# Optimization experiments

Measured on AMD Instinct MI355X. Metric: run time of the kernel, lower is better.

## Reference

```python
import jax, jax.numpy as jnp
import numpy as np

B, S, D = 2, 2048, 4096
H, KV, HD = 32, 8, 128          # query heads, kv heads, head_dim
N_REP = H // KV                 # GQA groups = 4
ROPE_THETA = 1000000.0


def setup_inputs() -> dict:
    key = jax.random.key(0)
    ks = jax.random.split(key, 8)
    s = 0.02
    return {
        "hidden_states": jax.random.normal(ks[0], (B, S, D), jnp.float32),
        "position_ids": jnp.broadcast_to(jnp.arange(S, dtype=jnp.int32)[None, :], (B, S)),
        "wq": jax.random.normal(ks[1], (D, H * HD), jnp.float32) * s,
        "bq": jax.random.normal(ks[2], (H * HD,), jnp.float32) * s,
        "wk": jax.random.normal(ks[3], (D, KV * HD), jnp.float32) * s,
        "bk": jax.random.normal(ks[4], (KV * HD,), jnp.float32) * s,
        "wv": jax.random.normal(ks[5], (D, KV * HD), jnp.float32) * s,
        "bv": jax.random.normal(ks[6], (KV * HD,), jnp.float32) * s,
        "wo": jax.random.normal(ks[7], (H * HD, D), jnp.float32) * s,
    }


def _rope_cos_sin(position_ids, head_dim, theta):
    pos = position_ids.astype(jnp.float32)
    dim = head_dim // 2
    freqs = 1.0 / theta ** (jnp.arange(0, dim, dtype=jnp.float32) / dim)
    t = pos[..., None] * freqs[None, None, :]          # [B,S,dim]
    return jnp.cos(t)[..., None, :], jnp.sin(t)[..., None, :]  # [B,S,1,dim]


def _apply_rope(x, cos, sin):
    half = x.shape[-1] // 2
    x1, x2 = x[..., :half], x[..., half:]
    return jnp.concatenate([x1 * cos - x2 * sin, x1 * sin + x2 * cos], axis=-1)


def reference(hidden_states, position_ids, wq, bq, wk, bk, wv, bv, wo):
    q = (hidden_states @ wq + bq).reshape(B, S, H, HD)
    k = (hidden_states @ wk + bk).reshape(B, S, KV, HD)
    v = (hidden_states @ wv + bv).reshape(B, S, KV, HD)

    cos, sin = _rope_cos_sin(position_ids, HD, ROPE_THETA)
    q = _apply_rope(q, cos, sin)
    k = _apply_rope(k, cos, sin)

    # GQA: physically expand KV heads (adjacent repeats, matches repeat_kv)
    k = jnp.repeat(k, N_REP, axis=2)   # [B,S,H,HD]
    v = jnp.repeat(v, N_REP, axis=2)

    # causal bias (attention_mask defaults to all-ones, so only causal matters)
    neg = jnp.finfo(jnp.float32).min
    causal = jnp.tril(jnp.ones((S, S), dtype=bool))
    bias = jnp.where(causal, 0.0, neg).astype(jnp.float32)  # [S,S]

    scale = 1.0 / jnp.sqrt(jnp.float32(HD))
    scores = jnp.einsum("bqhd,bkhd->bhqk", q * scale, k) + bias[None, None]
    attn = jax.nn.softmax(scores, axis=-1)                  # [B,H,S,S]
    out = jnp.einsum("bhqk,bkhd->bqhd", attn, v)
    out = out.reshape(B, S, H * HD)
    return out @ wo
```

## Files before the change

kernel.cpp:

```cpp
#include <hip/hip_runtime.h>
#include <hip/hip_bf16.h>
#include <math.h>


typedef __bf16 bf16;
typedef __attribute__((ext_vector_type(8))) __bf16 bf16x8;
typedef __attribute__((ext_vector_type(4))) float f32x4;

__device__ __forceinline__ void glds16(const void* g, void* l) {
    __builtin_amdgcn_global_load_lds(
        (const __attribute__((address_space(1))) void*)g,
        (__attribute__((address_space(3))) void*)l, 16, 0, 0);
}

__global__ __launch_bounds__(256) void convert_kernel(
    const float* __restrict__ in, bf16* __restrict__ out)
{
    const size_t i0 = ((size_t)blockIdx.x * 256 + threadIdx.x) * 8;
    const float4 a = *(const float4*)(in + i0);
    const float4 b = *(const float4*)(in + i0 + 4);
    bf16x8 p;
    p[0] = (bf16)a.x; p[1] = (bf16)a.y; p[2] = (bf16)a.z; p[3] = (bf16)a.w;
    p[4] = (bf16)b.x; p[5] = (bf16)b.y; p[6] = (bf16)b.z; p[7] = (bf16)b.w;
    *(bf16x8*)(out + i0) = p;
}

__global__ __launch_bounds__(256) void transpose_conv_kernel(
    const float* __restrict__ in, bf16* __restrict__ out, int N)
{
    __shared__ bf16 tile[32 * 68];
    const int n0 = blockIdx.x * 32, k0 = blockIdx.y * 64;
    const int t = threadIdx.x;
    const int nn = t & 31, kk0 = (t >> 5) * 8;
#pragma unroll
    for (int j = 0; j < 8; ++j)
        tile[nn * 68 + kk0 + j] = (bf16)in[(size_t)(k0 + kk0 + j) * N + n0 + nn];
    __syncthreads();
    const int n2 = t >> 3, c = (t & 7) * 8;
    *(bf16x8*)(out + (size_t)(n0 + n2) * 4096 + k0 + c) = *(const bf16x8*)(&tile[n2 * 68 + c]);
}

template <int EPI, int AF32>
__global__ __launch_bounds__(256) void gemm_kernel(
    const float* __restrict__ A_f32, const bf16* __restrict__ A_bf16,
    const bf16* __restrict__ BqT, const bf16* __restrict__ BkT, const bf16* __restrict__ BvT,
    const float* __restrict__ b_q, const float* __restrict__ b_k, const float* __restrict__ b_v,
    bf16* __restrict__ q_out, bf16* __restrict__ kv_k, bf16* __restrict__ kv_v,
    float* __restrict__ f_out)
{
    constexpr int LDA = AF32 ? 34 : 32;
    __shared__ bf16 As[128 * LDA];
    __shared__ bf16 Bs[128 * 32];

    const int nt = blockIdx.x, mt = blockIdx.y;
    const int tid = threadIdx.x;
    const int wave = tid >> 6, lane = tid & 63;
    const int l15 = lane & 15, quad = lane >> 4;
    const int wm = (wave >> 1) * 64, wn = (wave & 1) * 64;

    const bf16* BT;
    const float* bias = nullptr;
    int sel = 0, ncol0;
    if (EPI == 0) {
        if (nt < 32)      { BT = BqT; bias = b_q; sel = 0; ncol0 = nt * 128; }
        else if (nt < 40) { BT = BkT; bias = b_k; sel = 1; ncol0 = (nt - 32) * 128; }
        else              { BT = BvT; bias = b_v; sel = 2; ncol0 = (nt - 40) * 128; }
    } else {
        BT = BqT; ncol0 = nt * 128;
    }
    const int row0 = mt * 128;

    const f32x4 vzero = {0.f, 0.f, 0.f, 0.f};
    f32x4 acc[4][4];
#pragma unroll
    for (int mi = 0; mi < 4; ++mi)
#pragma unroll
        for (int ni = 0; ni < 4; ++ni) acc[mi][ni] = vzero;

    const int a_row = tid >> 1, a_seg = (tid & 1) * 16;
    const int g_row = lane >> 2, g_seg = (lane & 3) * 8;

    for (int k0 = 0; k0 < 4096; k0 += 32) {
        if (AF32) {
            const float4* src = (const float4*)(A_f32 + (size_t)(row0 + a_row) * 4096 + k0 + a_seg);
            float4 f0 = src[0], f1 = src[1], f2 = src[2], f3 = src[3];
            bf16x8 p0, p1;
            p0[0] = (bf16)f0.x; p0[1] = (bf16)f0.y; p0[2] = (bf16)f0.z; p0[3] = (bf16)f0.w;
            p0[4] = (bf16)f1.x; p0[5] = (bf16)f1.y; p0[6] = (bf16)f1.z; p0[7] = (bf16)f1.w;
            p1[0] = (bf16)f2.x; p1[1] = (bf16)f2.y; p1[2] = (bf16)f2.z; p1[3] = (bf16)f2.w;
            p1[4] = (bf16)f3.x; p1[5] = (bf16)f3.y; p1[6] = (bf16)f3.z; p1[7] = (bf16)f3.w;
            *(bf16x8*)(&As[a_row * LDA + a_seg]) = p0;
            *(bf16x8*)(&As[a_row * LDA + a_seg + 8]) = p1;
        } else {
#pragma unroll
            for (int c = 0; c < 2; ++c)
                glds16(A_bf16 + (size_t)(row0 + wave * 32 + c * 16 + g_row) * 4096 + k0 + g_seg,
                       &As[(wave * 32 + c * 16) * 32]);
        }
#pragma unroll
        for (int c = 0; c < 2; ++c)
            glds16(BT + (size_t)(ncol0 + wave * 32 + c * 16 + g_row) * 4096 + k0 + g_seg,
                   &Bs[(wave * 32 + c * 16) * 32]);
        __syncthreads();

        bf16x8 af[4], bfv[4];
#pragma unroll
        for (int mi = 0; mi < 4; ++mi)
            af[mi] = *(const bf16x8*)(&As[(wm + mi * 16 + l15) * LDA + quad * 8]);
#pragma unroll
        for (int ni = 0; ni < 4; ++ni)
            bfv[ni] = *(const bf16x8*)(&Bs[(wn + ni * 16 + l15) * 32 + quad * 8]);
#pragma unroll
        for (int mi = 0; mi < 4; ++mi)
#pragma unroll
            for (int ni = 0; ni < 4; ++ni)
                acc[mi][ni] = __builtin_amdgcn_mfma_f32_16x16x32_bf16(af[mi], bfv[ni], acc[mi][ni], 0, 0, 0);
        __syncthreads();
    }

#pragma unroll
    for (int mi = 0; mi < 4; ++mi)
#pragma unroll
        for (int ni = 0; ni < 4; ++ni)
#pragma unroll
            for (int i = 0; i < 4; ++i) {
                const int gr = row0 + wm + mi * 16 + quad * 4 + i;
                const int gc = ncol0 + wn + ni * 16 + l15;
                float vv = acc[mi][ni][i];
                if (EPI == 1) {
                    f_out[(size_t)gr * 4096 + gc] = vv;
                } else {
                    vv += bias[gc];
                    if (sel == 0) {
                        q_out[(size_t)gr * 4096 + gc] = (bf16)vv;
                    } else {
                        bf16* dst = (sel == 1) ? kv_k : kv_v;
                        dst[(size_t)((gr >> 11) * 8 + (gc >> 7)) * 262144 +
                            (size_t)(gr & 2047) * 128 + (gc & 127)] = (bf16)vv;
                    }
                }
            }
}

__global__ __launch_bounds__(256) void rope_q_kernel(
    bf16* __restrict__ q, const int* __restrict__ pos_ids)
{
    const int idx = blockIdx.x * 256 + threadIdx.x;
    const int d = idx & 63, h = (idx >> 6) & 31, tok = idx >> 11;
    const float posv = (float)pos_ids[tok];
    const float fr = exp2f((float)d * (-19.931568569324174f / 64.f));
    float sn, cs;
    sincosf(posv * fr, &sn, &cs);
    bf16* xp = q + (size_t)tok * 4096 + h * 128 + d;
    const float x1 = (float)xp[0], x2 = (float)xp[64];
    const float scale = 0.08838834764831845f;
    xp[0]  = (bf16)((x1 * cs - x2 * sn) * scale);
    xp[64] = (bf16)((x1 * sn + x2 * cs) * scale);
}

__global__ __launch_bounds__(256) void rope_k_kernel(
    bf16* __restrict__ k, const int* __restrict__ pos_ids)
{
    const int idx = blockIdx.x * 256 + threadIdx.x;
    const int d = idx & 63, s = (idx >> 6) & 2047, bk = idx >> 17;
    const int b = bk >> 3;
    const float posv = (float)pos_ids[b * 2048 + s];
    const float fr = exp2f((float)d * (-19.931568569324174f / 64.f));
    float sn, cs;
    sincosf(posv * fr, &sn, &cs);
    bf16* xp = k + ((size_t)bk * 2048 + s) * 128 + d;
    const float x1 = (float)xp[0], x2 = (float)xp[64];
    xp[0]  = (bf16)(x1 * cs - x2 * sn);
    xp[64] = (bf16)(x1 * sn + x2 * cs);
}

__global__ __launch_bounds__(256) void attn_kernel(
    const bf16* __restrict__ q, const bf16* __restrict__ k,
    const bf16* __restrict__ v, bf16* __restrict__ o)
{
    __shared__ bf16 Ksl[64 * 136];
    __shared__ bf16 Vsl[128 * 72];
    __shared__ bf16 Psl[4 * 16 * 68];

    const int pair = blockIdx.x & 7;
    const int h  = (blockIdx.x >> 3) & 31;
    const int b  = blockIdx.x >> 8;
    const int kvh = h >> 2;
    const int tid = threadIdx.x;
    const int wave = tid >> 6, lane = tid & 63;
    const int l15 = lane & 15, quad = lane >> 4;

    const bf16* kbase = k + (size_t)(b * 8 + kvh) * 2048 * 128;
    const bf16* vbase = v + (size_t)(b * 8 + kvh) * 2048 * 128;

    const int kr = tid >> 2, ksg = (tid & 3) * 32;
    const f32x4 vzero = {0.f, 0.f, 0.f, 0.f};

#pragma unroll 1
    for (int phase = 0; phase < 2; ++phase) {
        const int qt = phase ? (15 - pair) : pair;
        const int qbase = qt * 128 + wave * 32;

        bf16x8 qf[2][4];
#pragma unroll
        for (int mi = 0; mi < 2; ++mi) {
            const bf16* qrow = q + ((size_t)(b * 2048 + qbase + mi * 16 + l15) * 32 + h) * 128;
#pragma unroll
            for (int kb = 0; kb < 4; ++kb)
                qf[mi][kb] = *(const bf16x8*)(qrow + kb * 32 + quad * 8);
        }

        f32x4 acc_o[2][8];
#pragma unroll
        for (int mi = 0; mi < 2; ++mi)
#pragma unroll
            for (int i = 0; i < 8; ++i) acc_o[mi][i] = vzero;
        float m_i[2][4], l_i[2][4];
#pragma unroll
        for (int mi = 0; mi < 2; ++mi)
#pragma unroll
            for (int i = 0; i < 4; ++i) { m_i[mi][i] = -INFINITY; l_i[mi][i] = 0.f; }

        const int nT = 2 * qt + 2;
        for (int t = 0; t < nT; ++t) {
            const int kv0 = t * 64;
            {
                const bf16x8* ks = (const bf16x8*)(kbase + (size_t)(kv0 + kr) * 128 + ksg);
                bf16x8* kd = (bf16x8*)(&Ksl[kr * 136 + ksg]);
                kd[0] = ks[0]; kd[1] = ks[1]; kd[2] = ks[2]; kd[3] = ks[3];
            }
            {
                const bf16x8* vs = (const bf16x8*)(vbase + (size_t)(kv0 + lane) * 128 + wave * 32);
                bf16x8 w0 = vs[0], w1 = vs[1], w2 = vs[2], w3 = vs[3];
#pragma unroll
                for (int i = 0; i < 8; ++i) {
                    Vsl[(wave * 32 + i)      * 72 + lane] = w0[i];
                    Vsl[(wave * 32 + 8 + i)  * 72 + lane] = w1[i];
                    Vsl[(wave * 32 + 16 + i) * 72 + lane] = w2[i];
                    Vsl[(wave * 32 + 24 + i) * 72 + lane] = w3[i];
                }
            }
            __syncthreads();

            if (kv0 <= qbase + 31) {
                f32x4 sacc[2][4];
#pragma unroll
                for (int mi = 0; mi < 2; ++mi)
#pragma unroll
                    for (int nt = 0; nt < 4; ++nt) sacc[mi][nt] = vzero;
#pragma unroll
                for (int nt = 0; nt < 4; ++nt)
#pragma unroll
                    for (int kb = 0; kb < 4; ++kb) {
                        const bf16x8 kf = *(const bf16x8*)(&Ksl[(nt * 16 + l15) * 136 + kb * 32 + quad * 8]);
                        sacc[0][nt] = __builtin_amdgcn_mfma_f32_16x16x32_bf16(qf[0][kb], kf, sacc[0][nt], 0, 0, 0);
                        sacc[1][nt] = __builtin_amdgcn_mfma_f32_16x16x32_bf16(qf[1][kb], kf, sacc[1][nt], 0, 0, 0);
                    }

                bf16x8 pf[2][2];
#pragma unroll
                for (int mi = 0; mi < 2; ++mi) {
                    const int rb = qbase + mi * 16;
                    if (kv0 + 63 > rb) {
#pragma unroll
                        for (int nt = 0; nt < 4; ++nt) {
                            const int kvc = kv0 + nt * 16 + l15;
#pragma unroll
                            for (int i = 0; i < 4; ++i)
                                if (kvc > rb + quad * 4 + i) sacc[mi][nt][i] = -INFINITY;
                        }
                    }
                    float mt_[4];
#pragma unroll
                    for (int i = 0; i < 4; ++i)
                        mt_[i] = fmaxf(fmaxf(sacc[mi][0][i], sacc[mi][1][i]),
                                       fmaxf(sacc[mi][2][i], sacc[mi][3][i]));
#pragma unroll
                    for (int off = 1; off < 16; off <<= 1)
#pragma unroll
                        for (int i = 0; i < 4; ++i)
                            mt_[i] = fmaxf(mt_[i], __shfl_xor(mt_[i], off, 64));

                    float alpha[4];
#pragma unroll
                    for (int i = 0; i < 4; ++i) {
                        const float mnew = fmaxf(m_i[mi][i], mt_[i]);
                        alpha[i] = __expf(m_i[mi][i] - mnew);
                        m_i[mi][i] = mnew;
                    }
                    float rs[4] = {0.f, 0.f, 0.f, 0.f};
#pragma unroll
                    for (int nt = 0; nt < 4; ++nt)
#pragma unroll
                        for (int i = 0; i < 4; ++i) {
                            const float pv = __expf(sacc[mi][nt][i] - m_i[mi][i]);
                            rs[i] += pv;
                            Psl[wave * 1088 + (quad * 4 + i) * 68 + nt * 16 + l15] = (bf16)pv;
                        }
#pragma unroll
                    for (int off = 1; off < 16; off <<= 1)
#pragma unroll
                        for (int i = 0; i < 4; ++i)
                            rs[i] += __shfl_xor(rs[i], off, 64);
#pragma unroll
                    for (int i = 0; i < 4; ++i) l_i[mi][i] = l_i[mi][i] * alpha[i] + rs[i];
#pragma unroll
                    for (int dn = 0; dn < 8; ++dn)
#pragma unroll
                        for (int i = 0; i < 4; ++i) acc_o[mi][dn][i] *= alpha[i];
#pragma unroll
                    for (int k2 = 0; k2 < 2; ++k2)
                        pf[mi][k2] = *(const bf16x8*)(&Psl[wave * 1088 + l15 * 68 + k2 * 32 + quad * 8]);
                }

#pragma unroll
                for (int dn = 0; dn < 8; ++dn)
#pragma unroll
                    for (int k2 = 0; k2 < 2; ++k2) {
                        const bf16x8 vf = *(const bf16x8*)(&Vsl[(dn * 16 + l15) * 72 + k2 * 32 + quad * 8]);
                        acc_o[0][dn] = __builtin_amdgcn_mfma_f32_16x16x32_bf16(pf[0][k2], vf, acc_o[0][dn], 0, 0, 0);
                        acc_o[1][dn] = __builtin_amdgcn_mfma_f32_16x16x32_bf16(pf[1][k2], vf, acc_o[1][dn], 0, 0, 0);
                    }
            }
            __syncthreads();
        }

#pragma unroll
        for (int mi = 0; mi < 2; ++mi) {
            float inv[4];
#pragma unroll
            for (int i = 0; i < 4; ++i) inv[i] = 1.f / l_i[mi][i];
#pragma unroll
            for (int dn = 0; dn < 8; ++dn)
#pragma unroll
                for (int i = 0; i < 4; ++i) {
                    const int s = qbase + mi * 16 + quad * 4 + i;
                    o[(((size_t)b * 2048 + s) * 32 + h) * 128 + dn * 16 + l15] =
                        (bf16)(acc_o[mi][dn][i] * inv[i]);
                }
        }
    }
}

extern "C" void kernel_launch(void* const* d_in, const int* in_sizes, int n_in,
                              void* d_out, int out_size, void* d_ws, size_t ws_size,
                              hipStream_t stream)
{
    (void)in_sizes; (void)n_in; (void)out_size;
    const float* hidden = (const float*)d_in[0];
    const int*   pos    = (const int*)d_in[1];
    const float* wq     = (const float*)d_in[2];
    const float* bq_    = (const float*)d_in[3];
    const float* wk     = (const float*)d_in[4];
    const float* bk_    = (const float*)d_in[5];
    const float* wv     = (const float*)d_in[6];
    const float* bv_    = (const float*)d_in[7];
    const float* wo     = (const float*)d_in[8];
    float* out = (float*)d_out;

    char* ws = (char*)d_ws;
    bf16* wqT   = (bf16*)(ws);
    bf16* wkT   = (bf16*)(ws + 33554432);
    bf16* wvT   = (bf16*)(ws + 41943040);
    bf16* q_pre = (bf16*)(ws + 50331648);
    bf16* k_t   = (bf16*)(ws + 83886080);
    bf16* v_t   = (bf16*)(ws + 92274688);
    bf16* hid_b = (bf16*)(ws + 100663296);
    bf16* attn_o = wqT;
    bf16* woT    = q_pre;
    const bool have_hid = (ws_size >= 134217728);

    transpose_conv_kernel<<<dim3(128, 64), 256, 0, stream>>>(wq, wqT, 4096);
    transpose_conv_kernel<<<dim3(32, 64), 256, 0, stream>>>(wk, wkT, 1024);
    transpose_conv_kernel<<<dim3(32, 64), 256, 0, stream>>>(wv, wvT, 1024);

    if (have_hid) {
        convert_kernel<<<8192, 256, 0, stream>>>(hidden, hid_b);
        gemm_kernel<0, 0><<<dim3(48, 32), 256, 0, stream>>>(
            nullptr, hid_b, wqT, wkT, wvT, bq_, bk_, bv_, q_pre, k_t, v_t, nullptr);
    } else {
        gemm_kernel<0, 1><<<dim3(48, 32), 256, 0, stream>>>(
            hidden, nullptr, wqT, wkT, wvT, bq_, bk_, bv_, q_pre, k_t, v_t, nullptr);
    }

    rope_q_kernel<<<32768, 256, 0, stream>>>(q_pre, pos);
    rope_k_kernel<<<8192, 256, 0, stream>>>(k_t, pos);

    attn_kernel<<<512, 256, 0, stream>>>(q_pre, k_t, v_t, attn_o);

    transpose_conv_kernel<<<dim3(128, 64), 256, 0, stream>>>(wo, woT, 4096);

    gemm_kernel<1, 0><<<dim3(32, 32), 256, 0, stream>>>(
        nullptr, attn_o, woT, nullptr, nullptr, nullptr, nullptr, nullptr,
        nullptr, nullptr, nullptr, out);
}
```

Baseline: 921.0 us.

## Double-buffer K/V tiles with register prefetch and fuse both query-tile phases

Measured after the change: 953.6 us. +3.5%, slower.

```diff
diff --git a/kernel.cpp b/kernel.cpp
--- a/kernel.cpp
+++ b/kernel.cpp
@@ -178,9 +178,10 @@
     const bf16* __restrict__ q, const bf16* __restrict__ k,
     const bf16* __restrict__ v, bf16* __restrict__ o)
 {
-    __shared__ bf16 Ksl[64 * 136];
-    __shared__ bf16 Vsl[128 * 72];
-    __shared__ bf16 Psl[4 * 16 * 68];
+    constexpr int KSTR = 138, VSTR = 70, PSTR = 70;
+    __shared__ bf16 Ksl[2][64 * KSTR];
+    __shared__ bf16 Vsl[2][128 * VSTR];
+    __shared__ bf16 Psl[4 * 16 * PSTR];
 
     const int pair = blockIdx.x & 7;
     const int h  = (blockIdx.x >> 3) & 31;
@@ -190,141 +191,40 @@
     const int wave = tid >> 6, lane = tid & 63;
     const int l15 = lane & 15, quad = lane >> 4;
 
+    const int qt0 = pair, qt1 = 15 - pair;
+    const int nT0 = 2 * qt0 + 2, nT = nT0 + 2 * qt1 + 2;
+
     const bf16* kbase = k + (size_t)(b * 8 + kvh) * 2048 * 128;
     const bf16* vbase = v + (size_t)(b * 8 + kvh) * 2048 * 128;
 
     const int kr = tid >> 2, ksg = (tid & 3) * 32;
     const f32x4 vzero = {0.f, 0.f, 0.f, 0.f};
 
-#pragma unroll 1
-    for (int phase = 0; phase < 2; ++phase) {
-        const int qt = phase ? (15 - pair) : pair;
-        const int qbase = qt * 128 + wave * 32;
-
-        bf16x8 qf[2][4];
+    bf16x8 qf[2][4];
+    f32x4 acc_o[2][8];
+    float m_i[2][4], l_i[2][4];
+    int qbase = qt0 * 128 + wave * 32;
+
+    auto load_q = [&](int qt) {
+        const int qb = qt * 128 + wave * 32;
 #pragma unroll
         for (int mi = 0; mi < 2; ++mi) {
-            const bf16* qrow = q + ((size_t)(b * 2048 + qbase + mi * 16 + l15) * 32 + h) * 128;
+            const bf16* qrow = q + ((size_t)(b * 2048 + qb + mi * 16 + l15) * 32 + h) * 128;
 #pragma unroll
             for (int kb = 0; kb < 4; ++kb)
                 qf[mi][kb] = *(const bf16x8*)(qrow + kb * 32 + quad * 8);
         }
-
-        f32x4 acc_o[2][8];
-#pragma unroll
-        for (int mi = 0; mi < 2; ++mi)
+    };
+    auto reset_state = [&]() {
+#pragma unroll
+        for (int mi = 0; mi < 2; ++mi) {
 #pragma unroll
             for (int i = 0; i < 8; ++i) acc_o[mi][i] = vzero;
-        float m_i[2][4], l_i[2][4];
-#pragma unroll
-        for (int mi = 0; mi < 2; ++mi)
 #pragma unroll
             for (int i = 0; i < 4; ++i) { m_i[mi][i] = -INFINITY; l_i[mi][i] = 0.f; }
-
-        const int nT = 2 * qt + 2;
-        for (int t = 0; t < nT; ++t) {
-            const int kv0 = t * 64;
-            {
-                const bf16x8* ks = (const bf16x8*)(kbase + (size_t)(kv0 + kr) * 128 + ksg);
-                bf16x8* kd = (bf16x8*)(&Ksl[kr * 136 + ksg]);
-                kd[0] = ks[0]; kd[1] = ks[1]; kd[2] = ks[2]; kd[3] = ks[3];
-            }
-            {
-                const bf16x8* vs = (const bf16x8*)(vbase + (size_t)(kv0 + lane) * 128 + wave * 32);
-                bf16x8 w0 = vs[0], w1 = vs[1], w2 = vs[2], w3 = vs[3];
-#pragma unroll
-                for (int i = 0; i < 8; ++i) {
-                    Vsl[(wave * 32 + i)      * 72 + lane] = w0[i];
-                    Vsl[(wave * 32 + 8 + i)  * 72 + lane] = w1[i];
-                    Vsl[(wave * 32 + 16 + i) * 72 + lane] = w2[i];
-                    Vsl[(wave * 32 + 24 + i) * 72 + lane] = w3[i];
-                }
-            }
-            __syncthreads();
-
-            if (kv0 <= qbase + 31) {
-                f32x4 sacc[2][4];
-#pragma unroll
-                for (int mi = 0; mi < 2; ++mi)
-#pragma unroll
-                    for (int nt = 0; nt < 4; ++nt) sacc[mi][nt] = vzero;
-#pragma unroll
-                for (int nt = 0; nt < 4; ++nt)
-#pragma unroll
-                    for (int kb = 0; kb < 4; ++kb) {
-                        const bf16x8 kf = *(const bf16x8*)(&Ksl[(nt * 16 + l15) * 136 + kb * 32 + quad * 8]);
-                        sacc[0][nt] = __builtin_amdgcn_mfma_f32_16x16x32_bf16(qf[0][kb], kf, sacc[0][nt], 0, 0, 0);
-                        sacc[1][nt] = __builtin_amdgcn_mfma_f32_16x16x32_bf16(qf[1][kb], kf, sacc[1][nt], 0, 0, 0);
-                    }
-
-                bf16x8 pf[2][2];
-#pragma unroll
-                for (int mi = 0; mi < 2; ++mi) {
-                    const int rb = qbase + mi * 16;
-                    if (kv0 + 63 > rb) {
-#pragma unroll
-                        for (int nt = 0; nt < 4; ++nt) {
-                            const int kvc = kv0 + nt * 16 + l15;
-#pragma unroll
-                            for (int i = 0; i < 4; ++i)
-                                if (kvc > rb + quad * 4 + i) sacc[mi][nt][i] = -INFINITY;
-                        }
-                    }
-                    float mt_[4];
-#pragma unroll
-                    for (int i = 0; i < 4; ++i)
-                        mt_[i] = fmaxf(fmaxf(sacc[mi][0][i], sacc[mi][1][i]),
-                                       fmaxf(sacc[mi][2][i], sacc[mi][3][i]));
-#pragma unroll
-                    for (int off = 1; off < 16; off <<= 1)
-#pragma unroll
-                        for (int i = 0; i < 4; ++i)
-                            mt_[i] = fmaxf(mt_[i], __shfl_xor(mt_[i], off, 64));
-
-                    float alpha[4];
-#pragma unroll
-                    for (int i = 0; i < 4; ++i) {
-                        const float mnew = fmaxf(m_i[mi][i], mt_[i]);
-                        alpha[i] = __expf(m_i[mi][i] - mnew);
-                        m_i[mi][i] = mnew;
-                    }
-                    float rs[4] = {0.f, 0.f, 0.f, 0.f};
-#pragma unroll
-                    for (int nt = 0; nt < 4; ++nt)
-#pragma unroll
-                        for (int i = 0; i < 4; ++i) {
-                            const float pv = __expf(sacc[mi][nt][i] - m_i[mi][i]);
-                            rs[i] += pv;
-                            Psl[wave * 1088 + (quad * 4 + i) * 68 + nt * 16 + l15] = (bf16)pv;
-                        }
-#pragma unroll
-                    for (int off = 1; off < 16; off <<= 1)
-#pragma unroll
-                        for (int i = 0; i < 4; ++i)
-                            rs[i] += __shfl_xor(rs[i], off, 64);
-#pragma unroll
-                    for (int i = 0; i < 4; ++i) l_i[mi][i] = l_i[mi][i] * alpha[i] + rs[i];
-#pragma unroll
-                    for (int dn = 0; dn < 8; ++dn)
-#pragma unroll
-                        for (int i = 0; i < 4; ++i) acc_o[mi][dn][i] *= alpha[i];
-#pragma unroll
-                    for (int k2 = 0; k2 < 2; ++k2)
-                        pf[mi][k2] = *(const bf16x8*)(&Psl[wave * 1088 + l15 * 68 + k2 * 32 + quad * 8]);
-                }
-
-#pragma unroll
-                for (int dn = 0; dn < 8; ++dn)
-#pragma unroll
-                    for (int k2 = 0; k2 < 2; ++k2) {
-                        const bf16x8 vf = *(const bf16x8*)(&Vsl[(dn * 16 + l15) * 72 + k2 * 32 + quad * 8]);
-                        acc_o[0][dn] = __builtin_amdgcn_mfma_f32_16x16x32_bf16(pf[0][k2], vf, acc_o[0][dn], 0, 0, 0);
-                        acc_o[1][dn] = __builtin_amdgcn_mfma_f32_16x16x32_bf16(pf[1][k2], vf, acc_o[1][dn], 0, 0, 0);
-                    }
-            }
-            __syncthreads();
-        }
-
+        }
+    };
+    auto epilogue = [&]() {
 #pragma unroll
         for (int mi = 0; mi < 2; ++mi) {
             float inv[4];
@@ -339,7 +239,138 @@
                         (bf16)(acc_o[mi][dn][i] * inv[i]);
                 }
         }
+    };
+
+    bf16x8 kreg[4], vreg[4];
+    auto issue_loads = [&](int kv0) {
+        const bf16x8* ks = (const bf16x8*)(kbase + (size_t)(kv0 + kr) * 128 + ksg);
+        kreg[0] = ks[0]; kreg[1] = ks[1]; kreg[2] = ks[2]; kreg[3] = ks[3];
+        const bf16x8* vs = (const bf16x8*)(vbase + (size_t)(kv0 + lane) * 128 + wave * 32);
+        vreg[0] = vs[0]; vreg[1] = vs[1]; vreg[2] = vs[2]; vreg[3] = vs[3];
+    };
+    auto write_lds = [&](int buf) {
+        bf16x8* kd = (bf16x8*)(&Ksl[buf][kr * KSTR + ksg]);
+        kd[0] = kreg[0]; kd[1] = kreg[1]; kd[2] = kreg[2]; kd[3] = kreg[3];
+#pragma unroll
+        for (int i = 0; i < 8; ++i) {
+            Vsl[buf][(wave * 32 + i)      * VSTR + lane] = vreg[0][i];
+            Vsl[buf][(wave * 32 + 8 + i)  * VSTR + lane] = vreg[1][i];
+            Vsl[buf][(wave * 32 + 16 + i) * VSTR + lane] = vreg[2][i];
+            Vsl[buf][(wave * 32 + 24 + i) * VSTR + lane] = vreg[3][i];
+        }
+    };
+
+    issue_loads(0);
+    write_lds(0);
+    load_q(qt0);
+    reset_state();
+    __syncthreads();
+
+    int cur = 0;
+    for (int s = 0; s < nT; ++s) {
+        if (s + 1 < nT) {
+            const int nk = (s + 1 < nT0 ? s + 1 : s + 1 - nT0) * 64;
+            issue_loads(nk);
+        }
+        if (s == nT0) {
+            epilogue();
+            load_q(qt1);
+            reset_state();
+            qbase = qt1 * 128 + wave * 32;
+        }
+        const int kv0 = (s < nT0 ? s : s - nT0) * 64;
+
+        if (kv0 <= qbase + 31) {
+            f32x4 sacc[2][4];
+#pragma unroll
+            for (int mi = 0; mi < 2; ++mi)
+#pragma unroll
+                for (int nt = 0; nt < 4; ++nt) sacc[mi][nt] = vzero;
+            __builtin_amdgcn_s_setprio(1);
+#pragma unroll
+            for (int nt = 0; nt < 4; ++nt)
+#pragma unroll
+                for (int kb = 0; kb < 4; ++kb) {
+                    const bf16x8 kf = *(const bf16x8*)(&Ksl[cur][(nt * 16 + l15) * KSTR + kb * 32 + quad * 8]);
+                    sacc[0][nt] = __builtin_amdgcn_mfma_f32_16x16x32_bf16(qf[0][kb], kf, sacc[0][nt], 0, 0, 0);
+                    sacc[1][nt] = __builtin_amdgcn_mfma_f32_16x16x32_bf16(qf[1][kb], kf, sacc[1][nt], 0, 0, 0);
+                }
+            __builtin_amdgcn_s_setprio(0);
+
+            bf16x8 pf[2][2];
+#pragma unroll
+            for (int mi = 0; mi < 2; ++mi) {
+                const int rb = qbase + mi * 16;
+                if (kv0 + 63 > rb) {
+#pragma unroll
+                    for (int nt = 0; nt < 4; ++nt) {
+                        const int kvc = kv0 + nt * 16 + l15;
+#pragma unroll
+                        for (int i = 0; i < 4; ++i)
+                            if (kvc > rb + quad * 4 + i) sacc[mi][nt][i] = -INFINITY;
+                    }
+                }
+                float mt_[4];
+#pragma unroll
+                for (int i = 0; i < 4; ++i)
+                    mt_[i] = fmaxf(fmaxf(sacc[mi][0][i], sacc[mi][1][i]),
+                                   fmaxf(sacc[mi][2][i], sacc[mi][3][i]));
+#pragma unroll
+                for (int off = 1; off < 16; off <<= 1)
+#pragma unroll
+                    for (int i = 0; i < 4; ++i)
+                        mt_[i] = fmaxf(mt_[i], __shfl_xor(mt_[i], off, 64));
+
+                float alpha[4];
+#pragma unroll
+                for (int i = 0; i < 4; ++i) {
+                    const float mnew = fmaxf(m_i[mi][i], mt_[i]);
+                    alpha[i] = __expf(m_i[mi][i] - mnew);
+                    m_i[mi][i] = mnew;
+                }
+                float rs[4] = {0.f, 0.f, 0.f, 0.f};
+#pragma unroll
+                for (int nt = 0; nt < 4; ++nt)
+#pragma unroll
+                    for (int i = 0; i < 4; ++i) {
+                        const float pv = __expf(sacc[mi][nt][i] - m_i[mi][i]);
+                        rs[i] += pv;
+                        Psl[wave * (16 * PSTR) + (quad * 4 + i) * PSTR + nt * 16 + l15] = (bf16)pv;
+                    }
+#pragma unroll
+                for (int off = 1; off < 16; off <<= 1)
+#pragma unroll
+                    for (int i = 0; i < 4; ++i)
+                        rs[i] += __shfl_xor(rs[i], off, 64);
+#pragma unroll
+                for (int i = 0; i < 4; ++i) l_i[mi][i] = l_i[mi][i] * alpha[i] + rs[i];
+#pragma unroll
+                for (int dn = 0; dn < 8; ++dn)
+#pragma unroll
+                    for (int i = 0; i < 4; ++i) acc_o[mi][dn][i] *= alpha[i];
+#pragma unroll
+                for (int k2 = 0; k2 < 2; ++k2)
+                    pf[mi][k2] = *(const bf16x8*)(&Psl[wave * (16 * PSTR) + l15 * PSTR + k2 * 32 + quad * 8]);
+            }
+
+            __builtin_amdgcn_s_setprio(1);
+#pragma unroll
+            for (int dn = 0; dn < 8; ++dn)
+#pragma unroll
+                for (int k2 = 0; k2 < 2; ++k2) {
+                    const bf16x8 vf = *(const bf16x8*)(&Vsl[cur][(dn * 16 + l15) * VSTR + k2 * 32 + quad * 8]);
+                    acc_o[0][dn] = __builtin_amdgcn_mfma_f32_16x16x32_bf16(pf[0][k2], vf, acc_o[0][dn], 0, 0, 0);
+                    acc_o[1][dn] = __builtin_amdgcn_mfma_f32_16x16x32_bf16(pf[1][k2], vf, acc_o[1][dn], 0, 0, 0);
+                }
+            __builtin_amdgcn_s_setprio(0);
+        }
+
+        if (s + 1 < nT) write_lds(cur ^ 1);
+        __syncthreads();
+        cur ^= 1;
     }
+
+    epilogue();
 }
 
 extern "C" void kernel_launch(void* const* d_in, const int* in_sizes, int n_in,
```

## Transpose QK^T MFMA so softmax rows are lane-local, with lazy rescaling

Applied to the files above, without the earlier changes.

Result: faster. 872.5 us (-5.3%).

```diff
diff --git a/kernel.cpp b/kernel.cpp
--- a/kernel.cpp
+++ b/kernel.cpp
@@ -11,6 +11,12 @@
     __builtin_amdgcn_global_load_lds(
         (const __attribute__((address_space(1))) void*)g,
         (__attribute__((address_space(3))) void*)l, 16, 0, 0);
+}
+
+__device__ __forceinline__ unsigned cvt_pk_bf16(float lo, float hi) {
+    unsigned r;
+    asm("v_cvt_pk_bf16_f32 %0, %1, %2" : "=v"(r) : "v"(lo), "v"(hi));
+    return r;
 }
 
 __global__ __launch_bounds__(256) void convert_kernel(
@@ -215,11 +221,8 @@
         for (int mi = 0; mi < 2; ++mi)
 #pragma unroll
             for (int i = 0; i < 8; ++i) acc_o[mi][i] = vzero;
-        float m_i[2][4], l_i[2][4];
-#pragma unroll
-        for (int mi = 0; mi < 2; ++mi)
-#pragma unroll
-            for (int i = 0; i < 4; ++i) { m_i[mi][i] = -INFINITY; l_i[mi][i] = 0.f; }
+        float m_i[2] = {-INFINITY, -INFINITY};
+        float l_i[2] = {0.f, 0.f};
 
         const int nT = 2 * qt + 2;
         for (int t = 0; t < nT; ++t) {
@@ -248,14 +251,16 @@
                 for (int mi = 0; mi < 2; ++mi)
 #pragma unroll
                     for (int nt = 0; nt < 4; ++nt) sacc[mi][nt] = vzero;
+                __builtin_amdgcn_s_setprio(1);
 #pragma unroll
                 for (int nt = 0; nt < 4; ++nt)
 #pragma unroll
                     for (int kb = 0; kb < 4; ++kb) {
                         const bf16x8 kf = *(const bf16x8*)(&Ksl[(nt * 16 + l15) * 136 + kb * 32 + quad * 8]);
-                        sacc[0][nt] = __builtin_amdgcn_mfma_f32_16x16x32_bf16(qf[0][kb], kf, sacc[0][nt], 0, 0, 0);
-                        sacc[1][nt] = __builtin_amdgcn_mfma_f32_16x16x32_bf16(qf[1][kb], kf, sacc[1][nt], 0, 0, 0);
-                    }
+                        sacc[0][nt] = __builtin_amdgcn_mfma_f32_16x16x32_bf16(kf, qf[0][kb], sacc[0][nt], 0, 0, 0);
+                        sacc[1][nt] = __builtin_amdgcn_mfma_f32_16x16x32_bf16(kf, qf[1][kb], sacc[1][nt], 0, 0, 0);
+                    }
+                __builtin_amdgcn_s_setprio(0);
 
                 bf16x8 pf[2][2];
 #pragma unroll
@@ -264,55 +269,62 @@
                     if (kv0 + 63 > rb) {
 #pragma unroll
                         for (int nt = 0; nt < 4; ++nt) {
-                            const int kvc = kv0 + nt * 16 + l15;
+                            const int kvr = kv0 + nt * 16 + quad * 4;
 #pragma unroll
                             for (int i = 0; i < 4; ++i)
-                                if (kvc > rb + quad * 4 + i) sacc[mi][nt][i] = -INFINITY;
+                                if (kvr + i > rb + l15) sacc[mi][nt][i] = -INFINITY;
                         }
                     }
-                    float mt_[4];
-#pragma unroll
-                    for (int i = 0; i < 4; ++i)
-                        mt_[i] = fmaxf(fmaxf(sacc[mi][0][i], sacc[mi][1][i]),
-                                       fmaxf(sacc[mi][2][i], sacc[mi][3][i]));
-#pragma unroll
-                    for (int off = 1; off < 16; off <<= 1)
+                    float tm;
+                    {
+                        f32x4 m4;
 #pragma unroll
                         for (int i = 0; i < 4; ++i)
-                            mt_[i] = fmaxf(mt_[i], __shfl_xor(mt_[i], off, 64));
-
-                    float alpha[4];
-#pragma unroll
-                    for (int i = 0; i < 4; ++i) {
-                        const float mnew = fmaxf(m_i[mi][i], mt_[i]);
-                        alpha[i] = __expf(m_i[mi][i] - mnew);
-                        m_i[mi][i] = mnew;
-                    }
-                    float rs[4] = {0.f, 0.f, 0.f, 0.f};
+                            m4[i] = fmaxf(fmaxf(sacc[mi][0][i], sacc[mi][1][i]),
+                                          fmaxf(sacc[mi][2][i], sacc[mi][3][i]));
+                        tm = fmaxf(fmaxf(m4[0], m4[1]), fmaxf(m4[2], m4[3]));
+                        tm = fmaxf(tm, __shfl_xor(tm, 16, 64));
+                        tm = fmaxf(tm, __shfl_xor(tm, 32, 64));
+                    }
+                    if (!__all(tm - m_i[mi] <= 8.f)) {
+                        const float mnew = fmaxf(m_i[mi], tm);
+                        const float alpha = __expf(m_i[mi] - mnew);
+                        m_i[mi] = mnew;
+                        l_i[mi] *= alpha;
+                        float aw[4];
+#pragma unroll
+                        for (int i = 0; i < 4; ++i)
+                            aw[i] = __shfl(alpha, quad * 4 + i, 16);
+#pragma unroll
+                        for (int dn = 0; dn < 8; ++dn)
+#pragma unroll
+                            for (int i = 0; i < 4; ++i) acc_o[mi][dn][i] *= aw[i];
+                    }
+                    float p[4][4];
+                    float rs = 0.f;
 #pragma unroll
                     for (int nt = 0; nt < 4; ++nt)
 #pragma unroll
                         for (int i = 0; i < 4; ++i) {
-                            const float pv = __expf(sacc[mi][nt][i] - m_i[mi][i]);
-                            rs[i] += pv;
-                            Psl[wave * 1088 + (quad * 4 + i) * 68 + nt * 16 + l15] = (bf16)pv;
+                            p[nt][i] = __expf(sacc[mi][nt][i] - m_i[mi]);
+                            rs += p[nt][i];
                         }
-#pragma unroll
-                    for (int off = 1; off < 16; off <<= 1)
-#pragma unroll
-                        for (int i = 0; i < 4; ++i)
-                            rs[i] += __shfl_xor(rs[i], off, 64);
-#pragma unroll
-                    for (int i = 0; i < 4; ++i) l_i[mi][i] = l_i[mi][i] * alpha[i] + rs[i];
-#pragma unroll
-                    for (int dn = 0; dn < 8; ++dn)
-#pragma unroll
-                        for (int i = 0; i < 4; ++i) acc_o[mi][dn][i] *= alpha[i];
+                    rs += __shfl_xor(rs, 16, 64);
+                    rs += __shfl_xor(rs, 32, 64);
+                    l_i[mi] += rs;
+#pragma unroll
+                    for (int nt = 0; nt < 4; ++nt) {
+                        uint2 w;
+                        w.x = cvt_pk_bf16(p[nt][0], p[nt][1]);
+                        w.y = cvt_pk_bf16(p[nt][2], p[nt][3]);
+                        *(uint2*)(&Psl[wave * 1088 + l15 * 68 + nt * 16 + quad * 4]) = w;
+                    }
 #pragma unroll
                     for (int k2 = 0; k2 < 2; ++k2)
                         pf[mi][k2] = *(const bf16x8*)(&Psl[wave * 1088 + l15 * 68 + k2 * 32 + quad * 8]);
                 }
 
+                __builtin_amdgcn_s_setprio(1);
 #pragma unroll
                 for (int dn = 0; dn < 8; ++dn)
 #pragma unroll
@@ -321,22 +333,25 @@
                         acc_o[0][dn] = __builtin_amdgcn_mfma_f32_16x16x32_bf16(pf[0][k2], vf, acc_o[0][dn], 0, 0, 0);
                         acc_o[1][dn] = __builtin_amdgcn_mfma_f32_16x16x32_bf16(pf[1][k2], vf, acc_o[1][dn], 0, 0, 0);
                     }
+                __builtin_amdgcn_s_setprio(0);
             }
             __syncthreads();
         }
 
 #pragma unroll
         for (int mi = 0; mi < 2; ++mi) {
-            float inv[4];
-#pragma unroll
-            for (int i = 0; i < 4; ++i) inv[i] = 1.f / l_i[mi][i];
+            const float inv = 1.f / l_i[mi];
+            float invw[4];
+#pragma unroll
+            for (int i = 0; i < 4; ++i)
+                invw[i] = __shfl(inv, quad * 4 + i, 16);
 #pragma unroll
             for (int dn = 0; dn < 8; ++dn)
 #pragma unroll
                 for (int i = 0; i < 4; ++i) {
                     const int s = qbase + mi * 16 + quad * 4 + i;
                     o[(((size_t)b * 2048 + s) * 32 + h) * 128 + dn * 16 + l15] =
-                        (bf16)(acc_o[mi][dn][i] * inv[i]);
+                        (bf16)(acc_o[mi][dn][i] * invw[i]);
                 }
         }
     }
```
